# Optimization experiments

Measured on AMD Instinct MI355X. Metric: run time of the kernel, lower is better.

The kernel has to match this reference:

```python
import jax, jax.numpy as jnp
import numpy as np

B, H, S, D = 4, 16, 2048, 128

def setup_inputs() -> dict:
    key = jax.random.key(0)
    kq, kk, kv = jax.random.split(key, 3)
    Q = jax.random.normal(kq, (B, H, S, D), dtype=jnp.float32)
    K = jax.random.normal(kk, (B, H, S, D), dtype=jnp.float32)
    V = jax.random.normal(kv, (B, H, S, D), dtype=jnp.float32)
    # causal mask: True = attend (lower triangle incl. diagonal)
    mask = jnp.tril(jnp.ones((S, S), dtype=jnp.bool_))[None, None, :, :]
    return {"Q": Q, "K": K, "V": V, "mask": mask}

def reference(Q, K, V, mask):
    d_k = Q.shape[-1]
    scale = 1.0 / jnp.sqrt(jnp.asarray(d_k, Q.dtype))
    # [B,H,Sq,Sk] score matrix (naive, materialized, as in the original)
    scores = jnp.einsum('bhqd,bhkd->bhqk', Q, K) * scale
    scores = jnp.where(mask, scores, jnp.asarray(-1e9, scores.dtype))
    attn = jax.nn.softmax(scores, axis=-1)
    return jnp.einsum('bhqk,bhkd->bhqd', attn, V)
```

## Files before the change

### kernel.cpp

```cpp
#include <hip/hip_runtime.h>
#include <hip/hip_bf16.h>

constexpr int S_LEN = 2048;
constexpr int D_DIM = 128;

typedef __attribute__((ext_vector_type(8))) short short8;
typedef __attribute__((ext_vector_type(4))) float f32x4;

__device__ inline short f2bf(float f) {
    unsigned u = __builtin_bit_cast(unsigned, f);
    u += 0x7fffu + ((u >> 16) & 1u);
    return (short)(u >> 16);
}

constexpr int SK_STRIDE  = 136;
constexpr int SVT_STRIDE = 72;
constexpr int SP_STRIDE  = 72;

__global__ __launch_bounds__(256, 4)
void fa_causal_kernel(const float* __restrict__ Q, const float* __restrict__ K,
                      const float* __restrict__ V, float* __restrict__ Out) {
    __shared__ short sK[64 * SK_STRIDE];
    __shared__ short sVt[128 * SVT_STRIDE];
    short* sP = sK;

    const int tid  = threadIdx.x;
    const int wid  = tid >> 6;
    const int lane = tid & 63;
    const int quad = lane >> 4;
    const int l16  = lane & 15;

    const int x  = blockIdx.x;
    const int bh = blockIdx.y;
    const size_t base = (size_t)bh * S_LEN * D_DIM;
    const float scale = 0.08838834764831845f;

    for (int pi = 0; pi < 2; ++pi) {
        const int qt = (pi == 0) ? (31 - x) : x;
        const int q0 = qt * 64;

        short8 q_frag[4];
        {
            const float* qp = Q + base + (size_t)(q0 + wid * 16 + l16) * D_DIM;
            for (int kk = 0; kk < 4; ++kk) {
                const int d0 = kk * 32 + quad * 8;
                float4 a = *reinterpret_cast<const float4*>(qp + d0);
                float4 b = *reinterpret_cast<const float4*>(qp + d0 + 4);
                short8 f;
                f[0]=f2bf(a.x*scale); f[1]=f2bf(a.y*scale);
                f[2]=f2bf(a.z*scale); f[3]=f2bf(a.w*scale);
                f[4]=f2bf(b.x*scale); f[5]=f2bf(b.y*scale);
                f[6]=f2bf(b.z*scale); f[7]=f2bf(b.w*scale);
                q_frag[kk] = f;
            }
        }

        f32x4 o_acc[8];
        for (int i = 0; i < 8; ++i) o_acc[i] = f32x4{0.f,0.f,0.f,0.f};
        float m_i[4], l_i[4];
        for (int r = 0; r < 4; ++r) { m_i[r] = -1e30f; l_i[r] = 0.f; }

        for (int kt = 0; kt <= qt; ++kt) {
            for (int it = 0; it < 4; ++it) {
                const int idx = (it * 256 + tid) * 8;
                const int key = idx >> 7, d = idx & 127;
                const float* kp = K + base + (size_t)(kt * 64 + key) * D_DIM + d;
                float4 a = *reinterpret_cast<const float4*>(kp);
                float4 b = *reinterpret_cast<const float4*>(kp + 4);
                short8 f;
                f[0]=f2bf(a.x); f[1]=f2bf(a.y); f[2]=f2bf(a.z); f[3]=f2bf(a.w);
                f[4]=f2bf(b.x); f[5]=f2bf(b.y); f[6]=f2bf(b.z); f[7]=f2bf(b.w);
                *reinterpret_cast<short8*>(&sK[key * SK_STRIDE + d]) = f;
            }
            for (int it = 0; it < 4; ++it) {
                const int idx = (it * 256 + tid) * 8;
                const int key = idx >> 7, d = idx & 127;
                const int kc = key >> 3, kw = key & 7;
                const float* vp = V + base + (size_t)(kt * 64 + key) * D_DIM + d;
                float4 a = *reinterpret_cast<const float4*>(vp);
                float4 b = *reinterpret_cast<const float4*>(vp + 4);
                float vals[8] = {a.x,a.y,a.z,a.w,b.x,b.y,b.z,b.w};
                const int rc = (d >> 3) & 7;
                const int cs = (kc ^ rc) * 8 + kw;
                for (int j = 0; j < 8; ++j)
                    sVt[(d + j) * SVT_STRIDE + cs] = f2bf(vals[j]);
            }
            __syncthreads();

            f32x4 s_acc[4];
            for (int ct = 0; ct < 4; ++ct) {
                f32x4 acc = f32x4{0.f,0.f,0.f,0.f};
                for (int kk = 0; kk < 4; ++kk) {
                    short8 kf = *reinterpret_cast<const short8*>(
                        &sK[(ct * 16 + l16) * SK_STRIDE + kk * 32 + quad * 8]);
                    acc = __builtin_amdgcn_mfma_f32_16x16x32_bf16(q_frag[kk], kf, acc, 0, 0, 0);
                }
                s_acc[ct] = acc;
            }

            if (kt == qt) {
                for (int ct = 0; ct < 4; ++ct) {
                    const int kg = ct * 16 + l16;
                    for (int r = 0; r < 4; ++r)
                        if (kg > wid * 16 + quad * 4 + r) s_acc[ct][r] = -1e30f;
                }
            }

            float tm[4];
            for (int r = 0; r < 4; ++r)
                tm[r] = fmaxf(fmaxf(s_acc[0][r], s_acc[1][r]),
                              fmaxf(s_acc[2][r], s_acc[3][r]));
            for (int off = 1; off < 16; off <<= 1)
                for (int r = 0; r < 4; ++r)
                    tm[r] = fmaxf(tm[r], __shfl_xor(tm[r], off));
            float alpha[4], m_new[4], rs[4];
            for (int r = 0; r < 4; ++r) {
                m_new[r] = fmaxf(m_i[r], tm[r]);
                alpha[r] = __expf(m_i[r] - m_new[r]);
                rs[r] = 0.f;
            }
            for (int ct = 0; ct < 4; ++ct)
                for (int r = 0; r < 4; ++r) {
                    float p = __expf(s_acc[ct][r] - m_new[r]);
                    s_acc[ct][r] = p;
                    rs[r] += p;
                }
            for (int off = 1; off < 16; off <<= 1)
                for (int r = 0; r < 4; ++r)
                    rs[r] += __shfl_xor(rs[r], off);
            for (int r = 0; r < 4; ++r) {
                l_i[r] = alpha[r] * l_i[r] + rs[r];
                m_i[r] = m_new[r];
            }
            for (int nt = 0; nt < 8; ++nt)
                for (int r = 0; r < 4; ++r)
                    o_acc[nt][r] *= alpha[r];

            __syncthreads();

            for (int ct = 0; ct < 4; ++ct)
                for (int r = 0; r < 4; ++r) {
                    const int row = wid * 16 + quad * 4 + r;
                    const int col = ct * 16 + l16;
                    sP[row * SP_STRIDE + (((col >> 3) ^ ((row >> 2) & 7)) << 3) + (col & 7)]
                        = f2bf(s_acc[ct][r]);
                }

            {
                const int prow = wid * 16 + l16;
                const int pxr  = (prow >> 2) & 7;
                for (int nt = 0; nt < 8; ++nt) {
                    const int vrow = nt * 16 + l16;
                    const int vxr  = (vrow >> 3) & 7;
                    for (int k2 = 0; k2 < 2; ++k2) {
                        const int chunk = k2 * 4 + quad;
                        short8 pf = *reinterpret_cast<const short8*>(
                            &sP[prow * SP_STRIDE + ((chunk ^ pxr) << 3)]);
                        short8 vf = *reinterpret_cast<const short8*>(
                            &sVt[vrow * SVT_STRIDE + ((chunk ^ vxr) << 3)]);
                        o_acc[nt] = __builtin_amdgcn_mfma_f32_16x16x32_bf16(pf, vf, o_acc[nt], 0, 0, 0);
                    }
                }
            }
            __syncthreads();
        }

        for (int nt = 0; nt < 8; ++nt)
            for (int r = 0; r < 4; ++r) {
                const int qrow = q0 + wid * 16 + quad * 4 + r;
                Out[base + (size_t)qrow * D_DIM + nt * 16 + l16] = o_acc[nt][r] / l_i[r];
            }
    }
}

extern "C" void kernel_launch(void* const* d_in, const int* in_sizes, int n_in,
                              void* d_out, int out_size, void* d_ws, size_t ws_size,
                              hipStream_t stream) {
    const float* Q = (const float*)d_in[0];
    const float* K = (const float*)d_in[1];
    const float* V = (const float*)d_in[2];
    float* Out = (float*)d_out;
    dim3 grid(16, 4 * 16);
    fa_causal_kernel<<<grid, 256, 0, stream>>>(Q, K, V, Out);
}
```

Measured before the change: 469.6 us.

## Use 128-row query tiles with 8 waves and register-prefetch next K/V tile

Blocks now hold 512 threads (8 waves) covering a 128-row query tile, so each K/V tile staged in shared memory is reused by twice as many query rows. The next K/V tile is loaded from global memory into registers while the current tile is being computed. The P buffer gets its own shared-memory array, which removes one barrier per iteration. The costs are more registers and shared memory per block, fewer blocks in the grid (512 instead of 1024), and a causal mask now applied to the last two key tiles. The diff also leaves dead empty mask loops behind.

```diff
diff --git a/kernel.cpp b/kernel.cpp
--- a/kernel.cpp
+++ b/kernel.cpp
@@ -17,12 +17,12 @@
 constexpr int SVT_STRIDE = 72;
 constexpr int SP_STRIDE  = 72;
 
-__global__ __launch_bounds__(256, 4)
+__global__ __launch_bounds__(512, 4)
 void fa_causal_kernel(const float* __restrict__ Q, const float* __restrict__ K,
                       const float* __restrict__ V, float* __restrict__ Out) {
-    __shared__ short sK[64 * SK_STRIDE];
+    __shared__ short sK [64  * SK_STRIDE];
     __shared__ short sVt[128 * SVT_STRIDE];
-    short* sP = sK;
+    __shared__ short sP [128 * SP_STRIDE];
 
     const int tid  = threadIdx.x;
     const int wid  = tid >> 6;
@@ -36,8 +36,9 @@
     const float scale = 0.08838834764831845f;
 
     for (int pi = 0; pi < 2; ++pi) {
-        const int qt = (pi == 0) ? (31 - x) : x;
-        const int q0 = qt * 64;
+        const int qt  = (pi == 0) ? (15 - x) : x;
+        const int q0  = qt * 128;
+        const int nkt = 2 * qt + 2;
 
         short8 q_frag[4];
         {
@@ -60,32 +61,49 @@
         float m_i[4], l_i[4];
         for (int r = 0; r < 4; ++r) { m_i[r] = -1e30f; l_i[r] = 0.f; }
 
-        for (int kt = 0; kt <= qt; ++kt) {
-            for (int it = 0; it < 4; ++it) {
-                const int idx = (it * 256 + tid) * 8;
-                const int key = idx >> 7, d = idx & 127;
-                const float* kp = K + base + (size_t)(kt * 64 + key) * D_DIM + d;
-                float4 a = *reinterpret_cast<const float4*>(kp);
-                float4 b = *reinterpret_cast<const float4*>(kp + 4);
-                short8 f;
-                f[0]=f2bf(a.x); f[1]=f2bf(a.y); f[2]=f2bf(a.z); f[3]=f2bf(a.w);
-                f[4]=f2bf(b.x); f[5]=f2bf(b.y); f[6]=f2bf(b.z); f[7]=f2bf(b.w);
-                *reinterpret_cast<short8*>(&sK[key * SK_STRIDE + d]) = f;
-            }
-            for (int it = 0; it < 4; ++it) {
-                const int idx = (it * 256 + tid) * 8;
-                const int key = idx >> 7, d = idx & 127;
-                const int kc = key >> 3, kw = key & 7;
-                const float* vp = V + base + (size_t)(kt * 64 + key) * D_DIM + d;
-                float4 a = *reinterpret_cast<const float4*>(vp);
-                float4 b = *reinterpret_cast<const float4*>(vp + 4);
-                float vals[8] = {a.x,a.y,a.z,a.w,b.x,b.y,b.z,b.w};
-                const int rc = (d >> 3) & 7;
-                const int cs = (kc ^ rc) * 8 + kw;
-                for (int j = 0; j < 8; ++j)
-                    sVt[(d + j) * SVT_STRIDE + cs] = f2bf(vals[j]);
-            }
-            __syncthreads();
+        int s_key[2], s_d[2];
+        for (int it = 0; it < 2; ++it) {
+            const int idx = (it * 512 + tid) * 8;
+            s_key[it] = idx >> 7;
+            s_d[it]   = idx & 127;
+        }
+
+        float4 kpre[2][2], vpre[2][2];
+
+        for (int it = 0; it < 2; ++it) {
+            const float* kp = K + base + (size_t)s_key[it] * D_DIM + s_d[it];
+            const float* vp = V + base + (size_t)s_key[it] * D_DIM + s_d[it];
+            kpre[it][0] = *reinterpret_cast<const float4*>(kp);
+            kpre[it][1] = *reinterpret_cast<const float4*>(kp + 4);
+            vpre[it][0] = *reinterpret_cast<const float4*>(vp);
+            vpre[it][1] = *reinterpret_cast<const float4*>(vp + 4);
+        }
+        for (int it = 0; it < 2; ++it) {
+            const int key = s_key[it], d = s_d[it];
+            short8 f;
+            f[0]=f2bf(kpre[it][0].x); f[1]=f2bf(kpre[it][0].y);
+            f[2]=f2bf(kpre[it][0].z); f[3]=f2bf(kpre[it][0].w);
+            f[4]=f2bf(kpre[it][1].x); f[5]=f2bf(kpre[it][1].y);
+            f[6]=f2bf(kpre[it][1].z); f[7]=f2bf(kpre[it][1].w);
+            *reinterpret_cast<short8*>(&sK[key * SK_STRIDE + d]) = f;
+            const int cs = (((key >> 3) ^ ((d >> 3) & 7)) << 3) + (key & 7);
+            float vals[8] = {vpre[it][0].x, vpre[it][0].y, vpre[it][0].z, vpre[it][0].w,
+                             vpre[it][1].x, vpre[it][1].y, vpre[it][1].z, vpre[it][1].w};
+            for (int j = 0; j < 8; ++j)
+                sVt[(d + j) * SVT_STRIDE + cs] = f2bf(vals[j]);
+        }
+        __syncthreads();
+
+        for (int kt = 0; kt < nkt; ++kt) {
+            const int ktn = (kt + 1 < nkt) ? (kt + 1) : kt;
+            for (int it = 0; it < 2; ++it) {
+                const float* kp = K + base + (size_t)(ktn * 64 + s_key[it]) * D_DIM + s_d[it];
+                const float* vp = V + base + (size_t)(ktn * 64 + s_key[it]) * D_DIM + s_d[it];
+                kpre[it][0] = *reinterpret_cast<const float4*>(kp);
+                kpre[it][1] = *reinterpret_cast<const float4*>(kp + 4);
+                vpre[it][0] = *reinterpret_cast<const float4*>(vp);
+                vpre[it][1] = *reinterpret_cast<const float4*>(vp + 4);
+            }
 
             f32x4 s_acc[4];
             for (int ct = 0; ct < 4; ++ct) {
@@ -98,11 +116,27 @@
                 s_acc[ct] = acc;
             }
 
-            if (kt == qt) {
+            if (kt >= nkt - 2) {
                 for (int ct = 0; ct < 4; ++ct) {
-                    const int kg = ct * 16 + l16;
+                    const int kg = kt * 64 + ct * 16 + l16;
+                    const int qg = wid * 16 + quad * 4;
                     for (int r = 0; r < 4; ++r)
-                        if (kg > wid * 16 + quad * 4 + r) s_acc[ct][r] = -1e30f;
+                        if (kg > qg + r + (q0 - q0)) {  }
+                }
+                for (int ct = 0; ct < 4; ++ct) {
+                    const int kg = kt * 64 + ct * 16 + l16;
+                    for (int r = 0; r < 4; ++r) {
+                        const int qg = 128 * 0 + wid * 16 + quad * 4 + r + (q0 - q0);
+                        if (kg > q0 - q0 + wid * 16 + quad * 4 + r + (q0 - kt * 0) - q0 + qg - qg)
+                        { }
+                    }
+                }
+                for (int ct = 0; ct < 4; ++ct) {
+                    const int kg_abs = kt * 64 + ct * 16 + l16;
+                    for (int r = 0; r < 4; ++r) {
+                        const int q_abs = q0 + wid * 16 + quad * 4 + r;
+                        if (kg_abs > q_abs) s_acc[ct][r] = -1e30f;
+                    }
                 }
             }
 
@@ -135,8 +169,6 @@
             for (int nt = 0; nt < 8; ++nt)
                 for (int r = 0; r < 4; ++r)
                     o_acc[nt][r] *= alpha[r];
-
-            __syncthreads();
 
             for (int ct = 0; ct < 4; ++ct)
                 for (int r = 0; r < 4; ++r) {
@@ -163,6 +195,24 @@
                 }
             }
             __syncthreads();
+
+            if (kt + 1 < nkt) {
+                for (int it = 0; it < 2; ++it) {
+                    const int key = s_key[it], d = s_d[it];
+                    short8 f;
+                    f[0]=f2bf(kpre[it][0].x); f[1]=f2bf(kpre[it][0].y);
+                    f[2]=f2bf(kpre[it][0].z); f[3]=f2bf(kpre[it][0].w);
+                    f[4]=f2bf(kpre[it][1].x); f[5]=f2bf(kpre[it][1].y);
+                    f[6]=f2bf(kpre[it][1].z); f[7]=f2bf(kpre[it][1].w);
+                    *reinterpret_cast<short8*>(&sK[key * SK_STRIDE + d]) = f;
+                    const int cs = (((key >> 3) ^ ((d >> 3) & 7)) << 3) + (key & 7);
+                    float vals[8] = {vpre[it][0].x, vpre[it][0].y, vpre[it][0].z, vpre[it][0].w,
+                                     vpre[it][1].x, vpre[it][1].y, vpre[it][1].z, vpre[it][1].w};
+                    for (int j = 0; j < 8; ++j)
+                        sVt[(d + j) * SVT_STRIDE + cs] = f2bf(vals[j]);
+                }
+                __syncthreads();
+            }
         }
 
         for (int nt = 0; nt < 8; ++nt)
@@ -180,6 +230,6 @@
     const float* K = (const float*)d_in[1];
     const float* V = (const float*)d_in[2];
     float* Out = (float*)d_out;
-    dim3 grid(16, 4 * 16);
-    fa_causal_kernel<<<grid, 256, 0, stream>>>(Q, K, V, Out);
+    dim3 grid(8, 4 * 16);
+    fa_causal_kernel<<<grid, 512, 0, stream>>>(Q, K, V, Out);
 }
```

Result: slower. 550.8 us (+17.3%).

## Pre-convert K/V to swizzled bf16 tiles and stream them via async global-to-LDS loads

Applied to the files above, without the earlier changes.

A new preprocessing kernel converts K and V once to bf16, pre-transposing and swizzling V, and writes the tiles into the workspace. The main attention kernel then copies each K/V tile straight into LDS with global_load_lds, prefetching the next K tile during the PV step and the next V tile after it, with a separate sP buffer. This removes the repeated fp32 loads and conversions per query tile and halves global traffic per tile, at the cost of an extra launch, a workspace dependency, and more LDS, which may limit occupancy. A fallback keeps the old kernel when the workspace is too small.

```diff
diff --git a/kernel.cpp b/kernel.cpp
--- a/kernel.cpp
+++ b/kernel.cpp
@@ -3,26 +3,84 @@
 
 constexpr int S_LEN = 2048;
 constexpr int D_DIM = 128;
+constexpr int NBH   = 64;
+constexpr int NKT   = 32;
+constexpr size_t TILE_SHORTS = 64 * 128;
+constexpr size_t PAIR_SHORTS = 2 * TILE_SHORTS;
+constexpr size_t WS_NEEDED   = (size_t)NBH * NKT * PAIR_SHORTS * 2;
 
 typedef __attribute__((ext_vector_type(8))) short short8;
 typedef __attribute__((ext_vector_type(4))) float f32x4;
 
-__device__ inline short f2bf(float f) {
+__device__ __forceinline__ short f2bf(float f) {
     unsigned u = __builtin_bit_cast(unsigned, f);
     u += 0x7fffu + ((u >> 16) & 1u);
     return (short)(u >> 16);
 }
 
-constexpr int SK_STRIDE  = 136;
-constexpr int SVT_STRIDE = 72;
-constexpr int SP_STRIDE  = 72;
+__device__ __forceinline__ int kpos(int dc, int key) { return dc ^ (key & 15); }
+__device__ __forceinline__ int vpos(int kc, int d) {
+    return kc ^ ((d >> 3) & 7) ^ (d & 7);
+}
+
+__global__ __launch_bounds__(256)
+void preprocess_kv(const float* __restrict__ K, const float* __restrict__ V,
+                   short* __restrict__ ws) {
+    __shared__ short sv[128 * 64];
+    const int tid = threadIdx.x;
+    const int kt  = blockIdx.x;
+    const int bh  = blockIdx.y;
+    const size_t inbase = ((size_t)bh * S_LEN + (size_t)kt * 64) * D_DIM;
+    short* wk = ws + ((size_t)bh * NKT + kt) * PAIR_SHORTS;
+    short* wv = wk + TILE_SHORTS;
+
+    for (int it = 0; it < 4; ++it) {
+        const int idx = (it * 256 + tid) * 8;
+        const int key = idx >> 7, d = idx & 127;
+        const float* kp = K + inbase + (size_t)key * D_DIM + d;
+        float4 a = *reinterpret_cast<const float4*>(kp);
+        float4 b = *reinterpret_cast<const float4*>(kp + 4);
+        short8 f;
+        f[0]=f2bf(a.x); f[1]=f2bf(a.y); f[2]=f2bf(a.z); f[3]=f2bf(a.w);
+        f[4]=f2bf(b.x); f[5]=f2bf(b.y); f[6]=f2bf(b.z); f[7]=f2bf(b.w);
+        *reinterpret_cast<short8*>(&wk[key * 128 + (kpos(d >> 3, key) << 3)]) = f;
+        const float* vp = V + inbase + (size_t)key * D_DIM + d;
+        float4 c = *reinterpret_cast<const float4*>(vp);
+        float4 e = *reinterpret_cast<const float4*>(vp + 4);
+        float vals[8] = {c.x,c.y,c.z,c.w,e.x,e.y,e.z,e.w};
+        for (int j = 0; j < 8; ++j) {
+            const int dr = d + j;
+            sv[dr * 64 + (vpos(key >> 3, dr) << 3) + (key & 7)] = f2bf(vals[j]);
+        }
+    }
+    __syncthreads();
+    for (int it = 0; it < 4; ++it) {
+        const int off = (it * 256 + tid) * 8;
+        *reinterpret_cast<short8*>(&wv[off]) =
+            *reinterpret_cast<const short8*>(&sv[off]);
+    }
+}
+
+__device__ __forceinline__ void async_copy_1k(const short* gsrc, short* ldst,
+                                              int lane) {
+    __builtin_amdgcn_global_load_lds(
+        (const __attribute__((address_space(1))) void*)(gsrc + lane * 8),
+        (__attribute__((address_space(3))) void*)ldst, 16, 0, 0);
+}
+__device__ __forceinline__ void dma_tile16k(const short* gsrc, short* ldst,
+                                            int wid, int lane) {
+    for (int i = 0; i < 4; ++i) {
+        const int s = wid * 4 + i;
+        async_copy_1k(gsrc + s * 512, ldst + s * 512, lane);
+    }
+}
 
 __global__ __launch_bounds__(256, 4)
-void fa_causal_kernel(const float* __restrict__ Q, const float* __restrict__ K,
-                      const float* __restrict__ V, float* __restrict__ Out) {
-    __shared__ short sK[64 * SK_STRIDE];
-    __shared__ short sVt[128 * SVT_STRIDE];
-    short* sP = sK;
+void fa_causal_main(const float* __restrict__ Q, const short* __restrict__ ws,
+                    float* __restrict__ Out) {
+    __shared__ short sK [64 * 128];
+    __shared__ short sVt[128 * 64];
+    __shared__ short sP [64 * 64];
 
     const int tid  = threadIdx.x;
     const int wid  = tid >> 6;
@@ -33,6 +91,7 @@
     const int x  = blockIdx.x;
     const int bh = blockIdx.y;
     const size_t base = (size_t)bh * S_LEN * D_DIM;
+    const short* tiles = ws + (size_t)bh * NKT * PAIR_SHORTS;
     const float scale = 0.08838834764831845f;
 
     for (int pi = 0; pi < 2; ++pi) {
@@ -60,6 +119,147 @@
         float m_i[4], l_i[4];
         for (int r = 0; r < 4; ++r) { m_i[r] = -1e30f; l_i[r] = 0.f; }
 
+        dma_tile16k(tiles, sK, wid, lane);
+        dma_tile16k(tiles + TILE_SHORTS, sVt, wid, lane);
+
+        for (int kt = 0; kt <= qt; ++kt) {
+            __syncthreads();
+
+            f32x4 s_acc[4];
+            for (int ct = 0; ct < 4; ++ct) {
+                const int key = ct * 16 + l16;
+                f32x4 acc = f32x4{0.f,0.f,0.f,0.f};
+                for (int kk = 0; kk < 4; ++kk) {
+                    short8 kf = *reinterpret_cast<const short8*>(
+                        &sK[key * 128 + (kpos(kk * 4 + quad, key) << 3)]);
+                    acc = __builtin_amdgcn_mfma_f32_16x16x32_bf16(q_frag[kk], kf, acc, 0, 0, 0);
+                }
+                s_acc[ct] = acc;
+            }
+
+            if (kt == qt) {
+                for (int ct = 0; ct < 4; ++ct) {
+                    const int kg = ct * 16 + l16;
+                    for (int r = 0; r < 4; ++r)
+                        if (kg > wid * 16 + quad * 4 + r) s_acc[ct][r] = -1e30f;
+                }
+            }
+
+            float tm[4];
+            for (int r = 0; r < 4; ++r)
+                tm[r] = fmaxf(fmaxf(s_acc[0][r], s_acc[1][r]),
+                              fmaxf(s_acc[2][r], s_acc[3][r]));
+            for (int off = 1; off < 16; off <<= 1)
+                for (int r = 0; r < 4; ++r)
+                    tm[r] = fmaxf(tm[r], __shfl_xor(tm[r], off));
+            float alpha[4], m_new[4], rs[4];
+            for (int r = 0; r < 4; ++r) {
+                m_new[r] = fmaxf(m_i[r], tm[r]);
+                alpha[r] = __expf(m_i[r] - m_new[r]);
+                rs[r] = 0.f;
+            }
+            for (int ct = 0; ct < 4; ++ct)
+                for (int r = 0; r < 4; ++r) {
+                    float p = __expf(s_acc[ct][r] - m_new[r]);
+                    s_acc[ct][r] = p;
+                    rs[r] += p;
+                }
+            for (int off = 1; off < 16; off <<= 1)
+                for (int r = 0; r < 4; ++r)
+                    rs[r] += __shfl_xor(rs[r], off);
+            for (int r = 0; r < 4; ++r) {
+                l_i[r] = alpha[r] * l_i[r] + rs[r];
+                m_i[r] = m_new[r];
+            }
+            for (int nt = 0; nt < 8; ++nt)
+                for (int r = 0; r < 4; ++r)
+                    o_acc[nt][r] *= alpha[r];
+
+            __syncthreads();
+
+            if (kt < qt)
+                dma_tile16k(tiles + (size_t)(kt + 1) * PAIR_SHORTS, sK, wid, lane);
+
+            for (int ct = 0; ct < 4; ++ct)
+                for (int r = 0; r < 4; ++r) {
+                    const int row = wid * 16 + quad * 4 + r;
+                    const int col = ct * 16 + l16;
+                    sP[row * 64 + (((col >> 3) ^ (row & 7)) << 3) + (col & 7)]
+                        = f2bf(s_acc[ct][r]);
+                }
+
+            {
+                const int prow = wid * 16 + l16;
+                short8 pf[2];
+                for (int k2 = 0; k2 < 2; ++k2)
+                    pf[k2] = *reinterpret_cast<const short8*>(
+                        &sP[prow * 64 + (((k2 * 4 + quad) ^ (prow & 7)) << 3)]);
+                for (int nt = 0; nt < 8; ++nt) {
+                    const int vrow = nt * 16 + l16;
+                    for (int k2 = 0; k2 < 2; ++k2) {
+                        short8 vf = *reinterpret_cast<const short8*>(
+                            &sVt[vrow * 64 + (vpos(k2 * 4 + quad, vrow) << 3)]);
+                        o_acc[nt] = __builtin_amdgcn_mfma_f32_16x16x32_bf16(pf[k2], vf, o_acc[nt], 0, 0, 0);
+                    }
+                }
+            }
+
+            __syncthreads();
+
+            if (kt < qt)
+                dma_tile16k(tiles + (size_t)(kt + 1) * PAIR_SHORTS + TILE_SHORTS,
+                            sVt, wid, lane);
+        }
+
+        for (int nt = 0; nt < 8; ++nt)
+            for (int r = 0; r < 4; ++r) {
+                const int qrow = q0 + wid * 16 + quad * 4 + r;
+                Out[base + (size_t)qrow * D_DIM + nt * 16 + l16] = o_acc[nt][r] / l_i[r];
+            }
+    }
+}
+
+constexpr int SK_STRIDE  = 136;
+constexpr int SVT_STRIDE = 72;
+constexpr int SP_STRIDE  = 72;
+
+__global__ __launch_bounds__(256, 4)
+void fa_causal_fallback(const float* __restrict__ Q, const float* __restrict__ K,
+                        const float* __restrict__ V, float* __restrict__ Out) {
+    __shared__ short sK[64 * SK_STRIDE];
+    __shared__ short sVt[128 * SVT_STRIDE];
+    short* sP = sK;
+    const int tid  = threadIdx.x;
+    const int wid  = tid >> 6;
+    const int lane = tid & 63;
+    const int quad = lane >> 4;
+    const int l16  = lane & 15;
+    const int x  = blockIdx.x;
+    const int bh = blockIdx.y;
+    const size_t base = (size_t)bh * S_LEN * D_DIM;
+    const float scale = 0.08838834764831845f;
+    for (int pi = 0; pi < 2; ++pi) {
+        const int qt = (pi == 0) ? (31 - x) : x;
+        const int q0 = qt * 64;
+        short8 q_frag[4];
+        {
+            const float* qp = Q + base + (size_t)(q0 + wid * 16 + l16) * D_DIM;
+            for (int kk = 0; kk < 4; ++kk) {
+                const int d0 = kk * 32 + quad * 8;
+                float4 a = *reinterpret_cast<const float4*>(qp + d0);
+                float4 b = *reinterpret_cast<const float4*>(qp + d0 + 4);
+                short8 f;
+                f[0]=f2bf(a.x*scale); f[1]=f2bf(a.y*scale);
+                f[2]=f2bf(a.z*scale); f[3]=f2bf(a.w*scale);
+                f[4]=f2bf(b.x*scale); f[5]=f2bf(b.y*scale);
+                f[6]=f2bf(b.z*scale); f[7]=f2bf(b.w*scale);
+                q_frag[kk] = f;
+            }
+        }
+        f32x4 o_acc[8];
+        for (int i = 0; i < 8; ++i) o_acc[i] = f32x4{0.f,0.f,0.f,0.f};
+        float m_i[4], l_i[4];
+        for (int r = 0; r < 4; ++r) { m_i[r] = -1e30f; l_i[r] = 0.f; }
         for (int kt = 0; kt <= qt; ++kt) {
             for (int it = 0; it < 4; ++it) {
                 const int idx = (it * 256 + tid) * 8;
@@ -86,7 +286,6 @@
                     sVt[(d + j) * SVT_STRIDE + cs] = f2bf(vals[j]);
             }
             __syncthreads();
-
             f32x4 s_acc[4];
             for (int ct = 0; ct < 4; ++ct) {
                 f32x4 acc = f32x4{0.f,0.f,0.f,0.f};
@@ -97,7 +296,6 @@
                 }
                 s_acc[ct] = acc;
             }
-
             if (kt == qt) {
                 for (int ct = 0; ct < 4; ++ct) {
                     const int kg = ct * 16 + l16;
@@ -105,7 +303,6 @@
                         if (kg > wid * 16 + quad * 4 + r) s_acc[ct][r] = -1e30f;
                 }
             }
-
             float tm[4];
             for (int r = 0; r < 4; ++r)
                 tm[r] = fmaxf(fmaxf(s_acc[0][r], s_acc[1][r]),
@@ -135,9 +332,7 @@
             for (int nt = 0; nt < 8; ++nt)
                 for (int r = 0; r < 4; ++r)
                     o_acc[nt][r] *= alpha[r];
-
-            __syncthreads();
-
+            __syncthreads();
             for (int ct = 0; ct < 4; ++ct)
                 for (int r = 0; r < 4; ++r) {
                     const int row = wid * 16 + quad * 4 + r;
@@ -145,7 +340,6 @@
                     sP[row * SP_STRIDE + (((col >> 3) ^ ((row >> 2) & 7)) << 3) + (col & 7)]
                         = f2bf(s_acc[ct][r]);
                 }
-
             {
                 const int prow = wid * 16 + l16;
                 const int pxr  = (prow >> 2) & 7;
@@ -164,7 +358,6 @@
             }
             __syncthreads();
         }
-
         for (int nt = 0; nt < 8; ++nt)
             for (int r = 0; r < 4; ++r) {
                 const int qrow = q0 + wid * 16 + quad * 4 + r;
@@ -180,6 +373,12 @@
     const float* K = (const float*)d_in[1];
     const float* V = (const float*)d_in[2];
     float* Out = (float*)d_out;
-    dim3 grid(16, 4 * 16);
-    fa_causal_kernel<<<grid, 256, 0, stream>>>(Q, K, V, Out);
-}
+
+    if (ws_size >= WS_NEEDED) {
+        short* ws = (short*)d_ws;
+        preprocess_kv<<<dim3(NKT, NBH), 256, 0, stream>>>(K, V, ws);
+        fa_causal_main<<<dim3(16, NBH), 256, 0, stream>>>(Q, ws, Out);
+    } else {
+        fa_causal_fallback<<<dim3(16, NBH), 256, 0, stream>>>(Q, K, V, Out);
+    }
+}
```

New measurement: 433.0 us. 7.8% less time.
